# Optimization experiments

Measured on AMD Instinct MI355X. Metric: run time of the kernel, lower is better.

The kernel has to match this reference:

```python
import jax, jax.numpy as jnp
import numpy as np

B, N, C = 16, 4096, 512
FR = 2          # fr_ratio
NH = 8          # num_heads
CF = C // FR    # 256, q/k/v projection dim
HD = (C // NH) // FR  # 32, per-head dim after fr reduction
EPS = 1e-4


def _abs_clamp(t):
    # sign(t) * clamp(|t|, 1e-4, 1e4), as in the torch module's abs_clamp
    return jnp.sign(t) * jnp.clip(jnp.abs(t), 1e-4, 1e4)


def setup_inputs() -> dict:
    key = jax.random.key(0)
    ks = jax.random.split(key, 8)
    s = 0.02  # trunc_normal_(std=0.02) init scale
    return {
        "query": jax.random.normal(ks[0], (B, N, C), jnp.float32),
        "Wq": jax.random.normal(ks[1], (CF, C), jnp.float32) * s,
        "bq": jnp.zeros((CF,), jnp.float32),
        "Wk": jax.random.normal(ks[2], (CF, C), jnp.float32) * s,
        "bk": jnp.zeros((CF,), jnp.float32),
        "Wv": jax.random.normal(ks[3], (CF, C), jnp.float32) * s,
        "bv": jnp.zeros((CF,), jnp.float32),
        "Wo": jax.random.normal(ks[4], (C, CF), jnp.float32) * s,
        "bo": jnp.zeros((C,), jnp.float32),
        "Wse1": jax.random.normal(ks[5], (C // 2, C), jnp.float32) * s,
        "Wse2": jax.random.normal(ks[6], (C, C // 2), jnp.float32) * s,
        "H": 64,
        "W": 64,
    }


def reference(query, Wq, bq, Wk, bk, Wv, bv, Wo, bo, Wse1, Wse2, H, W):
    Bq, Nq, Cq = query.shape  # N == H*W
    # --- squeeze-excitation gate: mean over tokens -> 2-layer MLP -> sigmoid
    se = jnp.mean(query, axis=1)                                   # [B, C]
    se = jax.nn.sigmoid(jax.nn.relu(se @ Wse1.T) @ Wse2.T)         # [B, C]

    # --- q/k/v projections (sr_ratio=1: k/v from full-length query)
    q = jax.nn.relu(query @ Wq.T + bq).reshape(Bq, Nq, NH, HD)     # [B,N,h,d]
    k = jax.nn.relu(query @ Wk.T + bk).reshape(Bq, Nq, NH, HD)
    v = (query @ Wv.T + bv).reshape(Bq, Nq, NH, HD)

    # --- cosFormer-style 2D positional feature maps
    c = jnp.pi / 2
    idx = jnp.arange(Nq)
    a = (c * (idx // W).astype(query.dtype) / H)[None, :, None, None]  # row angle
    b = (c * (idx % W).astype(query.dtype) / W)[None, :, None, None]   # col angle
    q_ = jnp.concatenate([q * jnp.cos(a), q * jnp.sin(a),
                          q * jnp.cos(b), q * jnp.sin(b)], axis=-1)    # [B,N,h,4d]
    k_ = jnp.concatenate([k * jnp.cos(a), k * jnp.sin(a),
                          k * jnp.cos(b), k * jnp.sin(b)], axis=-1)    # sr_ratio=1 -> same angles

    # --- linear attention: kv state then q lookup, with abs-clamping
    kv = _abs_clamp(jnp.einsum('bnhf,bnhd->bhfd', k_, v))          # [B,h,4d,d]
    k_sum = jnp.sum(k_, axis=1, keepdims=True)                     # [B,1,h,4d]
    z = _abs_clamp(1.0 / (jnp.sum(q_ * k_sum, axis=-1) + EPS))     # [B,N,h]
    out = _abs_clamp(jnp.einsum('bnhf,bhfd->bnhd', q_, kv))        # [B,N,h,d]
    out = _abs_clamp(out * z[..., None])

    # --- output projection + SE residual gating
    out = _abs_clamp(out.reshape(Bq, Nq, CF) @ Wo.T + bo)          # [B,N,C]
    out = _abs_clamp(out + out * se[:, None, :])
    return out
```

## Files before the change

kernel.cpp:

```cpp
#include <hip/hip_runtime.h>
#include <math.h>

#define B_   16
#define N_   4096
#define C_   512
#define CF_  256
#define NH_  8
#define HD_  32
#define FHD_ 128
#define EPS_ 1e-4f
#define PI2F 1.5707963267948966f

typedef _Float16 half8 __attribute__((ext_vector_type(8)));
typedef _Float16 half4 __attribute__((ext_vector_type(4)));
typedef _Float16 half2v __attribute__((ext_vector_type(2)));
typedef float f32x4 __attribute__((ext_vector_type(4)));
typedef unsigned short u16x8 __attribute__((ext_vector_type(8)));

__device__ __forceinline__ float abs_clamp(float t) {
    float a = fminf(fmaxf(fabsf(t), 1e-4f), 1e4f);
    return t > 0.f ? a : (t < 0.f ? -a : 0.f);
}
__device__ __forceinline__ void gld16(const void* g, void* l) {
    __builtin_amdgcn_global_load_lds(
        (const __attribute__((address_space(1))) void*)g,
        (__attribute__((address_space(3))) void*)l, 16, 0, 0);
}

__global__ __launch_bounds__(256) void se_sum_kernel(const float* __restrict__ q,
                                                     float* __restrict__ sesum,
                                                     _Float16* __restrict__ q16) {
    int b = blockIdx.x, chunk = blockIdx.y;
    int t = threadIdx.x;
    int c0 = 2 * t;
    const float* p = q + ((size_t)b * N_ + (size_t)chunk * 256) * C_ + c0;
    _Float16* o = q16 + ((size_t)b * N_ + (size_t)chunk * 256) * C_ + c0;
    float a0 = 0.f, a1 = 0.f;
    for (int n = 0; n < 256; n++) {
        float2 v = *(const float2*)(p + (size_t)n * C_);
        a0 += v.x;
        a1 += v.y;
        half2v hv;
        hv[0] = (_Float16)v.x;
        hv[1] = (_Float16)v.y;
        *(half2v*)(o + (size_t)n * C_) = hv;
    }
    atomicAdd(&sesum[b * C_ + c0], a0);
    atomicAdd(&sesum[b * C_ + c0 + 1], a1);
}

__global__ __launch_bounds__(256) void se_gate_kernel(const float* __restrict__ sesum,
                                                      const float* __restrict__ Wse1,
                                                      const float* __restrict__ Wse2,
                                                      float* __restrict__ segate) {
    __shared__ float sm[C_];
    __shared__ float hm[C_ / 2];
    int b = blockIdx.x, t = threadIdx.x;
    sm[t]       = sesum[b * C_ + t]       * (1.f / N_);
    sm[t + 256] = sesum[b * C_ + t + 256] * (1.f / N_);
    __syncthreads();
    {
        const float* w = Wse1 + (size_t)t * C_;
        float acc = 0.f;
        for (int c2 = 0; c2 < C_; c2++) acc += sm[c2] * w[c2];
        hm[t] = fmaxf(acc, 0.f);
    }
    __syncthreads();
    for (int r = 0; r < 2; r++) {
        int c2 = t + r * 256;
        const float* w2 = Wse2 + (size_t)c2 * (C_ / 2);
        float a2 = 0.f;
        for (int j = 0; j < C_ / 2; j++) a2 += hm[j] * w2[j];
        segate[b * C_ + c2] = 1.f / (1.f + expf(-a2));
    }
}

__global__ __launch_bounds__(256) void convert_w(const float* __restrict__ Wq,
                                                 const float* __restrict__ Wk,
                                                 const float* __restrict__ Wv,
                                                 const float* __restrict__ Wo,
                                                 _Float16* __restrict__ wcat,
                                                 _Float16* __restrict__ wo16) {
    int i = blockIdx.x * 256 + threadIdx.x;
    if (i < 768 * 512) {
        int r = i >> 9, c = i & 511;
        float w = (r < 256) ? Wq[(size_t)r * 512 + c]
                : (r < 512) ? Wk[(size_t)(r - 256) * 512 + c]
                            : Wv[(size_t)(r - 512) * 512 + c];
        wcat[i] = (_Float16)w;
    } else {
        int j = i - 768 * 512;
        wo16[j] = (_Float16)Wo[j];
    }
}

__global__ __launch_bounds__(768) void gemm_qkv(
    const _Float16* __restrict__ A16, const _Float16* __restrict__ Bw,
    const float* __restrict__ bq, const float* __restrict__ bk, const float* __restrict__ bv,
    _Float16* __restrict__ O0, _Float16* __restrict__ O1, _Float16* __restrict__ O2) {
    constexpr int K = 512;
    constexpr int NITER = K / 32;

    __shared__ __align__(16) unsigned short As[2][128 * 32];
    __shared__ __align__(16) unsigned short Bs[2][384 * 32];

    const int t = threadIdx.x;
    const int Mb = blockIdx.y * 128;
    const int nrow0 = blockIdx.x * 384;

    const int lane = t & 63;
    const int wv = t >> 6;
    const int mq = (wv & 1) * 64;
    const int nq = (wv >> 1) * 64;
    const int mrow = lane & 15;
    const int kq = lane >> 4;
    const int fragoff = mrow * 32 + ((kq ^ ((mrow >> 1) & 3)) * 8);

    const unsigned char* bsrc0;
    const unsigned char* bsrc1;
    int boff0, boff1;
    {
        int cid0 = t, cid1 = t + 768;
        int m0 = cid0 >> 2, c0 = (cid0 & 3) ^ ((m0 >> 1) & 3);
        int m1 = cid1 >> 2, c1 = (cid1 & 3) ^ ((m1 >> 1) & 3);
        bsrc0 = (const unsigned char*)(Bw + (size_t)(nrow0 + m0) * K + c0 * 8);
        bsrc1 = (const unsigned char*)(Bw + (size_t)(nrow0 + m1) * K + c1 * 8);
        boff0 = cid0 * 8;
        boff1 = cid1 * 8;
    }
    const unsigned char* asrc = nullptr;
    int aoff = 0;
    if (t < 512) {
        int m0 = t >> 2, c0 = (t & 3) ^ ((m0 >> 1) & 3);
        asrc = (const unsigned char*)(A16 + (size_t)(Mb + m0) * K + c0 * 8);
        aoff = t * 8;
    }

    f32x4 acc[4][4];
#pragma unroll
    for (int mi = 0; mi < 4; mi++)
#pragma unroll
        for (int ni = 0; ni < 4; ni++) acc[mi][ni] = (f32x4){0.f, 0.f, 0.f, 0.f};

    if (t < 512) gld16(asrc, &As[0][aoff]);
    gld16(bsrc0, &Bs[0][boff0]);
    gld16(bsrc1, &Bs[0][boff1]);
    __syncthreads();

    int cur = 0;
#pragma unroll 1
    for (int it = 0; it < NITER; ++it) {
        if (it + 1 < NITER) {
            if (t < 512) gld16(asrc + (it + 1) * 64, &As[cur ^ 1][aoff]);
            gld16(bsrc0 + (it + 1) * 64, &Bs[cur ^ 1][boff0]);
            gld16(bsrc1 + (it + 1) * 64, &Bs[cur ^ 1][boff1]);
        }

        half8 ah[4], bh[4];
#pragma unroll
        for (int mi = 0; mi < 4; mi++)
            ah[mi] = *(const half8*)&As[cur][(mq + mi * 16) * 32 + fragoff];
#pragma unroll
        for (int ni = 0; ni < 4; ni++)
            bh[ni] = *(const half8*)&Bs[cur][(nq + ni * 16) * 32 + fragoff];
#pragma unroll
        for (int mi = 0; mi < 4; mi++)
#pragma unroll
            for (int ni = 0; ni < 4; ni++)
                acc[mi][ni] = __builtin_amdgcn_mfma_f32_16x16x32_f16(ah[mi], bh[ni], acc[mi][ni], 0, 0, 0);

        if (it + 1 < NITER) __syncthreads();
        cur ^= 1;
    }

#pragma unroll
    for (int ni = 0; ni < 4; ni++) {
        int gc = nrow0 + nq + ni * 16 + mrow;
        int mat = gc >> 8;
        int col = gc & 255;
        const float* bias = (mat == 0) ? bq : (mat == 1) ? bk : bv;
        _Float16* O = (mat == 0) ? O0 : (mat == 1) ? O1 : O2;
        float bb = bias[col];
#pragma unroll
        for (int mi = 0; mi < 4; mi++)
#pragma unroll
            for (int r = 0; r < 4; r++) {
                int m = Mb + mq + mi * 16 + kq * 4 + r;
                float v2 = acc[mi][ni][r] + bb;
                if (mat < 2) v2 = fmaxf(v2, 0.f);
                O[(size_t)m * CF_ + col] = (_Float16)v2;
            }
    }
}

__global__ __launch_bounds__(1024) void gemm_out(
    const _Float16* __restrict__ A16, const _Float16* __restrict__ Bw,
    const float* __restrict__ bo, const float* __restrict__ sg,
    float* __restrict__ Of) {
    constexpr int K = 256;
    constexpr int NITER = K / 32;

    __shared__ __align__(16) unsigned short As[2][128 * 32];
    __shared__ __align__(16) unsigned short Bs[2][512 * 32];

    const int t = threadIdx.x;
    const int Mb = blockIdx.x * 128;

    const int lane = t & 63;
    const int wv = t >> 6;
    const int mq = (wv & 1) * 64;
    const int nq = (wv >> 1) * 64;
    const int mrow = lane & 15;
    const int kq = lane >> 4;
    const int fragoff = mrow * 32 + ((kq ^ ((mrow >> 1) & 3)) * 8);

    const unsigned char* bsrc0;
    const unsigned char* bsrc1;
    int boff0, boff1;
    {
        int cid0 = t, cid1 = t + 1024;
        int m0 = cid0 >> 2, c0 = (cid0 & 3) ^ ((m0 >> 1) & 3);
        int m1 = cid1 >> 2, c1 = (cid1 & 3) ^ ((m1 >> 1) & 3);
        bsrc0 = (const unsigned char*)(Bw + (size_t)m0 * K + c0 * 8);
        bsrc1 = (const unsigned char*)(Bw + (size_t)m1 * K + c1 * 8);
        boff0 = cid0 * 8;
        boff1 = cid1 * 8;
    }
    const unsigned char* asrc = nullptr;
    int aoff = 0;
    if (t < 512) {
        int m0 = t >> 2, c0 = (t & 3) ^ ((m0 >> 1) & 3);
        asrc = (const unsigned char*)(A16 + (size_t)(Mb + m0) * K + c0 * 8);
        aoff = t * 8;
    }

    f32x4 acc[4][4];
#pragma unroll
    for (int mi = 0; mi < 4; mi++)
#pragma unroll
        for (int ni = 0; ni < 4; ni++) acc[mi][ni] = (f32x4){0.f, 0.f, 0.f, 0.f};

    if (t < 512) gld16(asrc, &As[0][aoff]);
    gld16(bsrc0, &Bs[0][boff0]);
    gld16(bsrc1, &Bs[0][boff1]);
    __syncthreads();

    int cur = 0;
#pragma unroll 1
    for (int it = 0; it < NITER; ++it) {
        if (it + 1 < NITER) {
            if (t < 512) gld16(asrc + (it + 1) * 64, &As[cur ^ 1][aoff]);
            gld16(bsrc0 + (it + 1) * 64, &Bs[cur ^ 1][boff0]);
            gld16(bsrc1 + (it + 1) * 64, &Bs[cur ^ 1][boff1]);
        }

        half8 ah[4], bh[4];
#pragma unroll
        for (int mi = 0; mi < 4; mi++)
            ah[mi] = *(const half8*)&As[cur][(mq + mi * 16) * 32 + fragoff];
#pragma unroll
        for (int ni = 0; ni < 4; ni++)
            bh[ni] = *(const half8*)&Bs[cur][(nq + ni * 16) * 32 + fragoff];
#pragma unroll
        for (int mi = 0; mi < 4; mi++)
#pragma unroll
            for (int ni = 0; ni < 4; ni++)
                acc[mi][ni] = __builtin_amdgcn_mfma_f32_16x16x32_f16(ah[mi], bh[ni], acc[mi][ni], 0, 0, 0);

        if (it + 1 < NITER) __syncthreads();
        cur ^= 1;
    }

    int b = Mb >> 12;
#pragma unroll
    for (int ni = 0; ni < 4; ni++) {
        int gc = nq + ni * 16 + mrow;
        float bb = bo[gc];
        float gv = sg[b * C_ + gc];
#pragma unroll
        for (int mi = 0; mi < 4; mi++)
#pragma unroll
            for (int r = 0; r < 4; r++) {
                int m = Mb + mq + mi * 16 + kq * 4 + r;
                float v2 = abs_clamp(acc[mi][ni][r] + bb);
                v2 = abs_clamp(v2 * (1.f + gv));
                Of[(size_t)m * C_ + gc] = v2;
            }
    }
}

__global__ __launch_bounds__(256) void kv_mfma_kernel(const _Float16* __restrict__ kin,
                                                      const _Float16* __restrict__ vin,
                                                      float* __restrict__ kvout,
                                                      float* __restrict__ ksum) {
    __shared__ __align__(16) unsigned short Ah[128 * 64];
    __shared__ __align__(16) unsigned short Bh[48 * 64];

    const int t = threadIdx.x;
    const int c8 = blockIdx.x;
    const int h = blockIdx.y, b = blockIdx.z;
    const int dp = t & 31;
    const int octet = t >> 5;

    if (t < 128) {
        int r = 32 + (t & 15);
        int oc = t >> 4;
        int off = r * 64 + (((oc ^ ((r >> 3) & 7)) & 7) * 8);
        unsigned short fill = (r == 32) ? (unsigned short)0x3C00 : (unsigned short)0;
        u16x8 z = {fill, fill, fill, fill, fill, fill, fill, fill};
        *(u16x8*)&Bh[off] = z;
    }

    float cbv[8], sbv[8];
#pragma unroll
    for (int i = 0; i < 8; i++) {
        float ang = (PI2F / 64.f) * (float)(octet * 8 + i);
        cbv[i] = cosf(ang);
        sbv[i] = sinf(ang);
    }

    const int lane = t & 63;
    const int wv = t >> 6;
    const int mrow = lane & 15;
    const int kq = lane >> 4;

    f32x4 acc[2][3];
#pragma unroll
    for (int mi = 0; mi < 2; mi++)
#pragma unroll
        for (int ni = 0; ni < 3; ni++) acc[mi][ni] = (f32x4){0.f, 0.f, 0.f, 0.f};

    int offA[4];
#pragma unroll
    for (int tvar = 0; tvar < 4; tvar++) {
        int f = tvar * 32 + dp;
        offA[tvar] = f * 64 + (((octet ^ ((f >> 3) & 7)) & 7) * 8);
    }
    const int offB = dp * 64 + (((octet ^ ((dp >> 3) & 7)) & 7) * 8);

#pragma unroll 1
    for (int ch = 0; ch < 8; ch++) {
        const int n0 = c8 * 512 + ch * 64;
        const int rrow = n0 >> 6;
        float aang = (PI2F / 64.f) * (float)rrow;
        float ca = cosf(aang), sa = sinf(aang);

        const _Float16* kp = kin + ((size_t)b * N_ + n0 + octet * 8) * CF_ + h * HD_ + dp;
        const _Float16* vp = vin + ((size_t)b * N_ + n0 + octet * 8) * CF_ + h * HD_ + dp;
        float kvl[8];
        _Float16 vvl[8];
#pragma unroll
        for (int i = 0; i < 8; i++) kvl[i] = (float)kp[(size_t)i * CF_];
#pragma unroll
        for (int i = 0; i < 8; i++) vvl[i] = vp[(size_t)i * CF_];

        __syncthreads();

#pragma unroll
        for (int tvar = 0; tvar < 4; tvar++) {
            half8 hv;
#pragma unroll
            for (int i = 0; i < 8; i++) {
                float val = kvl[i] * (tvar == 0 ? ca : tvar == 1 ? sa : tvar == 2 ? cbv[i] : sbv[i]);
                hv[i] = (_Float16)val;
            }
            *(half8*)&Ah[offA[tvar]] = hv;
        }
        {
            half8 hv;
#pragma unroll
            for (int i = 0; i < 8; i++) hv[i] = vvl[i];
            *(half8*)&Bh[offB] = hv;
        }
        __syncthreads();

#pragma unroll
        for (int s = 0; s < 2; s++) {
            half8 ah[2], bh[3];
            int koct = s * 4 + kq;
#pragma unroll
            for (int mi = 0; mi < 2; mi++) {
                int f = (wv * 2 + mi) * 16 + mrow;
                ah[mi] = *(const half8*)&Ah[f * 64 + (((koct ^ ((f >> 3) & 7)) & 7) * 8)];
            }
#pragma unroll
            for (int ni = 0; ni < 3; ni++) {
                int nr = ni * 16 + mrow;
                bh[ni] = *(const half8*)&Bh[nr * 64 + (((koct ^ ((nr >> 3) & 7)) & 7) * 8)];
            }
#pragma unroll
            for (int mi = 0; mi < 2; mi++)
#pragma unroll
                for (int ni = 0; ni < 3; ni++)
                    acc[mi][ni] = __builtin_amdgcn_mfma_f32_16x16x32_f16(ah[mi], bh[ni], acc[mi][ni], 0, 0, 0);
        }
    }

    float* kvp = kvout + (size_t)(b * NH_ + h) * FHD_ * HD_;
    float* ksp = ksum + (size_t)(b * NH_ + h) * FHD_;
#pragma unroll
    for (int mi = 0; mi < 2; mi++) {
        int mt = wv * 2 + mi;
#pragma unroll
        for (int r = 0; r < 4; r++) {
            int f = mt * 16 + kq * 4 + r;
            atomicAdd(&kvp[(size_t)f * HD_ + mrow], acc[mi][0][r]);
            atomicAdd(&kvp[(size_t)f * HD_ + 16 + mrow], acc[mi][1][r]);
            if (mrow == 0) atomicAdd(&ksp[f], acc[mi][2][r]);
        }
    }
}

__global__ __launch_bounds__(256) void attn_kernel(const _Float16* __restrict__ qbuf,
                                                   const float* __restrict__ kvin,
                                                   const float* __restrict__ ksum,
                                                   _Float16* __restrict__ ob) {
    int chunk = blockIdx.x;
    int h = blockIdx.y, b = blockIdx.z;
    int t = threadIdx.x;
    __shared__ float kvS[128][32];
    __shared__ float qS[128][33];
    __shared__ float tS[128][4];
    __shared__ float ksS[128];
    __shared__ float zS[128];
    int n0 = chunk * 128;

    const float* kvp = kvin + ((size_t)(b * NH_ + h)) * FHD_ * HD_;
#pragma unroll
    for (int r = 0; r < 16; r++) {
        int idx = t + r * 256;
        (&kvS[0][0])[idx] = abs_clamp(kvp[idx]);
    }
    if (t < 128) ksS[t] = ksum[(size_t)(b * NH_ + h) * FHD_ + t];
#pragma unroll
    for (int r = 0; r < 16; r++) {
        int idx = t + r * 256;
        int tok = idx >> 5, d = idx & 31;
        qS[tok][d] = (float)qbuf[((size_t)b * N_ + n0 + tok) * CF_ + h * HD_ + d];
    }
    if (t < 128) {
        int n = n0 + t;
        float ra = (float)(n >> 6), cb = (float)(n & 63);
        float aa = (PI2F * ra) / 64.0f;
        float ab = (PI2F * cb) / 64.0f;
        tS[t][0] = cosf(aa); tS[t][1] = sinf(aa);
        tS[t][2] = cosf(ab); tS[t][3] = sinf(ab);
    }
    __syncthreads();
    if (t < 128) {
        float s = 0.f;
        for (int f = 0; f < 128; f++) s += qS[t][f & 31] * tS[t][f >> 5] * ksS[f];
        zS[t] = abs_clamp(1.f / (s + EPS_));
    }
    __syncthreads();

    int tx = t & 7, ty = t >> 3;
    float acc[4][4];
#pragma unroll
    for (int u = 0; u < 4; u++)
#pragma unroll
        for (int w = 0; w < 4; w++) acc[u][w] = 0.f;

#pragma unroll
    for (int ti = 0; ti < 4; ti++) {
        float tr0 = tS[ty * 4 + 0][ti];
        float tr1 = tS[ty * 4 + 1][ti];
        float tr2 = tS[ty * 4 + 2][ti];
        float tr3 = tS[ty * 4 + 3][ti];
        for (int dd = 0; dd < 32; dd++) {
            int f = ti * 32 + dd;
            float4 kvv = *(const float4*)&kvS[f][tx * 4];
            float q0 = qS[ty * 4 + 0][dd] * tr0;
            float q1 = qS[ty * 4 + 1][dd] * tr1;
            float q2 = qS[ty * 4 + 2][dd] * tr2;
            float q3 = qS[ty * 4 + 3][dd] * tr3;
            acc[0][0] += q0 * kvv.x; acc[0][1] += q0 * kvv.y; acc[0][2] += q0 * kvv.z; acc[0][3] += q0 * kvv.w;
            acc[1][0] += q1 * kvv.x; acc[1][1] += q1 * kvv.y; acc[1][2] += q1 * kvv.z; acc[1][3] += q1 * kvv.w;
            acc[2][0] += q2 * kvv.x; acc[2][1] += q2 * kvv.y; acc[2][2] += q2 * kvv.z; acc[2][3] += q2 * kvv.w;
            acc[3][0] += q3 * kvv.x; acc[3][1] += q3 * kvv.y; acc[3][2] += q3 * kvv.z; acc[3][3] += q3 * kvv.w;
        }
    }

#pragma unroll
    for (int u = 0; u < 4; u++) {
        int tok = ty * 4 + u;
        float z = zS[tok];
        half4 hv;
        hv[0] = (_Float16)abs_clamp(abs_clamp(acc[u][0]) * z);
        hv[1] = (_Float16)abs_clamp(abs_clamp(acc[u][1]) * z);
        hv[2] = (_Float16)abs_clamp(abs_clamp(acc[u][2]) * z);
        hv[3] = (_Float16)abs_clamp(abs_clamp(acc[u][3]) * z);
        size_t base = ((size_t)b * N_ + n0 + tok) * CF_ + h * HD_ + tx * 4;
        *(half4*)&ob[base] = hv;
    }
}

extern "C" void kernel_launch(void* const* d_in, const int* in_sizes, int n_in,
                              void* d_out, int out_size, void* d_ws, size_t ws_size,
                              hipStream_t stream) {
    (void)in_sizes; (void)n_in; (void)out_size; (void)ws_size;
    const float* query = (const float*)d_in[0];
    const float* Wq = (const float*)d_in[1];
    const float* bq = (const float*)d_in[2];
    const float* Wk = (const float*)d_in[3];
    const float* bk = (const float*)d_in[4];
    const float* Wv = (const float*)d_in[5];
    const float* bv = (const float*)d_in[6];
    const float* Wo = (const float*)d_in[7];
    const float* bo = (const float*)d_in[8];
    const float* Wse1 = (const float*)d_in[9];
    const float* Wse2 = (const float*)d_in[10];
    float* out = (float*)d_out;

    unsigned char* ws = (unsigned char*)d_ws;
    const size_t MB = 1024ull * 1024ull;
    _Float16* q16 = (_Float16*)(ws + 0);
    _Float16* ob  = (_Float16*)(ws + 0);
    _Float16* qb = (_Float16*)(ws + 64 * MB);
    _Float16* kb = (_Float16*)(ws + 96 * MB);
    _Float16* vb = (_Float16*)(ws + 128 * MB);
    _Float16* wcat = (_Float16*)(ws + 160 * MB);
    _Float16* wo16 = (_Float16*)(ws + 160 * MB + 786432);
    float* kvb = (float*)(ws + 161 * MB);
    float* ksb = (float*)(ws + 163 * MB);
    float* ssb = (float*)(ws + 163 * MB + 65536);
    float* sgb = (float*)(ws + 163 * MB + 98304);

    hipMemsetAsync(kvb, 0, 2097152 + 65536 + 32768, stream);

    convert_w<<<2048, 256, 0, stream>>>(Wq, Wk, Wv, Wo, wcat, wo16);
    se_sum_kernel<<<dim3(B_, 16), 256, 0, stream>>>(query, ssb, q16);
    se_gate_kernel<<<B_, 256, 0, stream>>>(ssb, Wse1, Wse2, sgb);
    gemm_qkv<<<dim3(2, 512), 768, 0, stream>>>(q16, wcat, bq, bk, bv, qb, kb, vb);
    kv_mfma_kernel<<<dim3(8, NH_, B_), 256, 0, stream>>>(kb, vb, kvb, ksb);
    attn_kernel<<<dim3(32, NH_, B_), 256, 0, stream>>>(qb, kvb, ksb, ob);
    gemm_out<<<512, 1024, 0, stream>>>(ob, wo16, bo, sgb, out);
}
```

Measured before the change: 565.4 us.

## Rewrite attention lookup kernel with fp16 MFMA and fused k_sum normalizer

The per-chunk attention kernel now builds the positional-feature q tile in swizzled fp16 shared memory and runs q_·kv as 16x16x32 MFMA ops instead of scalar FP32 FMAs. k_sum is appended as an extra row of the B operand, so the z normalizer comes out of the same MFMA pass. The kv accumulator layout is transposed to d-major to match the new B operand loading. This removes the scalar FMA loop and the serial z reduction, at the cost of fp16 rounding on q_, kv and k_sum.

```diff
diff --git a/kernel.cpp b/kernel.cpp
--- a/kernel.cpp
+++ b/kernel.cpp
@@ -404,8 +404,8 @@
 #pragma unroll
         for (int r = 0; r < 4; r++) {
             int f = mt * 16 + kq * 4 + r;
-            atomicAdd(&kvp[(size_t)f * HD_ + mrow], acc[mi][0][r]);
-            atomicAdd(&kvp[(size_t)f * HD_ + 16 + mrow], acc[mi][1][r]);
+            atomicAdd(&kvp[(size_t)mrow * FHD_ + f], acc[mi][0][r]);
+            atomicAdd(&kvp[(size_t)(16 + mrow) * FHD_ + f], acc[mi][1][r]);
             if (mrow == 0) atomicAdd(&ksp[f], acc[mi][2][r]);
         }
     }
@@ -415,83 +415,126 @@
                                                    const float* __restrict__ kvin,
                                                    const float* __restrict__ ksum,
                                                    _Float16* __restrict__ ob) {
-    int chunk = blockIdx.x;
-    int h = blockIdx.y, b = blockIdx.z;
-    int t = threadIdx.x;
-    __shared__ float kvS[128][32];
-    __shared__ float qS[128][33];
-    __shared__ float tS[128][4];
-    __shared__ float ksS[128];
+    __shared__ __align__(16) unsigned short Aq[128 * 128];
+    __shared__ __align__(16) unsigned short Bk[48 * 128];
     __shared__ float zS[128];
-    int n0 = chunk * 128;
-
-    const float* kvp = kvin + ((size_t)(b * NH_ + h)) * FHD_ * HD_;
-#pragma unroll
-    for (int r = 0; r < 16; r++) {
-        int idx = t + r * 256;
-        (&kvS[0][0])[idx] = abs_clamp(kvp[idx]);
-    }
-    if (t < 128) ksS[t] = ksum[(size_t)(b * NH_ + h) * FHD_ + t];
-#pragma unroll
-    for (int r = 0; r < 16; r++) {
-        int idx = t + r * 256;
-        int tok = idx >> 5, d = idx & 31;
-        qS[tok][d] = (float)qbuf[((size_t)b * N_ + n0 + tok) * CF_ + h * HD_ + d];
-    }
-    if (t < 128) {
-        int n = n0 + t;
-        float ra = (float)(n >> 6), cb = (float)(n & 63);
-        float aa = (PI2F * ra) / 64.0f;
-        float ab = (PI2F * cb) / 64.0f;
-        tS[t][0] = cosf(aa); tS[t][1] = sinf(aa);
-        tS[t][2] = cosf(ab); tS[t][3] = sinf(ab);
+
+    const int chunk = blockIdx.x;
+    const int h = blockIdx.y, b = blockIdx.z;
+    const int t = threadIdx.x;
+    const int n0 = chunk * 128;
+
+    {
+        const float* kvp = kvin + ((size_t)(b * NH_ + h)) * (HD_ * FHD_);
+        int d = t >> 3;
+        int c0 = (t & 7) * 2;
+#pragma unroll
+        for (int cc = 0; cc < 2; cc++) {
+            int c = c0 + cc;
+            const float* src = kvp + (size_t)d * FHD_ + c * 8;
+            half8 hv;
+#pragma unroll
+            for (int i = 0; i < 8; i++) hv[i] = (_Float16)abs_clamp(src[i]);
+            *(half8*)&Bk[d * 128 + ((c ^ (d & 7)) * 8)] = hv;
+        }
+        if (t < 16) {
+            const float* ks = ksum + ((size_t)(b * NH_ + h)) * FHD_ + t * 8;
+            half8 hv;
+#pragma unroll
+            for (int i = 0; i < 8; i++) hv[i] = (_Float16)ks[i];
+            *(half8*)&Bk[32 * 128 + (t * 8)] = hv;
+        } else {
+            int idx = t - 16;
+            int r = 33 + (idx >> 4), c = idx & 15;
+            half8 z = {};
+            *(half8*)&Bk[r * 128 + ((c ^ (r & 7)) * 8)] = z;
+        }
+    }
+    {
+        int tok = t >> 1, hf = t & 1;
+        int n = n0 + tok;
+        const _Float16* qp = qbuf + ((size_t)b * N_ + n) * CF_ + h * HD_;
+        half8 q0 = *(const half8*)(qp + 0);
+        half8 q1 = *(const half8*)(qp + 8);
+        half8 q2 = *(const half8*)(qp + 16);
+        half8 q3 = *(const half8*)(qp + 24);
+        float f0, f1;
+        if (hf == 0) {
+            float aa = (PI2F / 64.f) * (float)(n >> 6);
+            f0 = cosf(aa); f1 = sinf(aa);
+        } else {
+            float ab = (PI2F / 64.f) * (float)(n & 63);
+            f0 = cosf(ab); f1 = sinf(ab);
+        }
+#pragma unroll
+        for (int ti = 0; ti < 2; ti++) {
+            float fac = ti ? f1 : f0;
+#pragma unroll
+            for (int dc = 0; dc < 4; dc++) {
+                half8 qv = (dc == 0) ? q0 : (dc == 1) ? q1 : (dc == 2) ? q2 : q3;
+                half8 hv;
+#pragma unroll
+                for (int i = 0; i < 8; i++) hv[i] = (_Float16)((float)qv[i] * fac);
+                int c = hf * 8 + ti * 4 + dc;
+                *(half8*)&Aq[tok * 128 + ((c ^ (tok & 7)) * 8)] = hv;
+            }
+        }
     }
     __syncthreads();
-    if (t < 128) {
-        float s = 0.f;
-        for (int f = 0; f < 128; f++) s += qS[t][f & 31] * tS[t][f >> 5] * ksS[f];
-        zS[t] = abs_clamp(1.f / (s + EPS_));
+
+    const int lane = t & 63;
+    const int wv = t >> 6;
+    const int mrow = lane & 15;
+    const int kq = lane >> 4;
+
+    f32x4 acc[2][3];
+#pragma unroll
+    for (int mi = 0; mi < 2; mi++)
+#pragma unroll
+        for (int ni = 0; ni < 3; ni++) acc[mi][ni] = (f32x4){0.f, 0.f, 0.f, 0.f};
+
+#pragma unroll
+    for (int ks = 0; ks < 4; ks++) {
+        half8 ah[2], bh[3];
+        int cpos = ks * 4 + kq;
+#pragma unroll
+        for (int mi = 0; mi < 2; mi++) {
+            int row = wv * 32 + mi * 16 + mrow;
+            ah[mi] = *(const half8*)&Aq[row * 128 + ((cpos ^ (row & 7)) * 8)];
+        }
+#pragma unroll
+        for (int ni = 0; ni < 3; ni++) {
+            int row = ni * 16 + mrow;
+            bh[ni] = *(const half8*)&Bk[row * 128 + ((cpos ^ (row & 7)) * 8)];
+        }
+#pragma unroll
+        for (int mi = 0; mi < 2; mi++)
+#pragma unroll
+            for (int ni = 0; ni < 3; ni++)
+                acc[mi][ni] = __builtin_amdgcn_mfma_f32_16x16x32_f16(ah[mi], bh[ni], acc[mi][ni], 0, 0, 0);
+    }
+
+    if (mrow == 0) {
+#pragma unroll
+        for (int mi = 0; mi < 2; mi++)
+#pragma unroll
+            for (int r = 0; r < 4; r++)
+                zS[wv * 32 + mi * 16 + kq * 4 + r] = acc[mi][2][r];
     }
     __syncthreads();
 
-    int tx = t & 7, ty = t >> 3;
-    float acc[4][4];
-#pragma unroll
-    for (int u = 0; u < 4; u++)
-#pragma unroll
-        for (int w = 0; w < 4; w++) acc[u][w] = 0.f;
-
-#pragma unroll
-    for (int ti = 0; ti < 4; ti++) {
-        float tr0 = tS[ty * 4 + 0][ti];
-        float tr1 = tS[ty * 4 + 1][ti];
-        float tr2 = tS[ty * 4 + 2][ti];
-        float tr3 = tS[ty * 4 + 3][ti];
-        for (int dd = 0; dd < 32; dd++) {
-            int f = ti * 32 + dd;
-            float4 kvv = *(const float4*)&kvS[f][tx * 4];
-            float q0 = qS[ty * 4 + 0][dd] * tr0;
-            float q1 = qS[ty * 4 + 1][dd] * tr1;
-            float q2 = qS[ty * 4 + 2][dd] * tr2;
-            float q3 = qS[ty * 4 + 3][dd] * tr3;
-            acc[0][0] += q0 * kvv.x; acc[0][1] += q0 * kvv.y; acc[0][2] += q0 * kvv.z; acc[0][3] += q0 * kvv.w;
-            acc[1][0] += q1 * kvv.x; acc[1][1] += q1 * kvv.y; acc[1][2] += q1 * kvv.z; acc[1][3] += q1 * kvv.w;
-            acc[2][0] += q2 * kvv.x; acc[2][1] += q2 * kvv.y; acc[2][2] += q2 * kvv.z; acc[2][3] += q2 * kvv.w;
-            acc[3][0] += q3 * kvv.x; acc[3][1] += q3 * kvv.y; acc[3][2] += q3 * kvv.z; acc[3][3] += q3 * kvv.w;
-        }
-    }
-
-#pragma unroll
-    for (int u = 0; u < 4; u++) {
-        int tok = ty * 4 + u;
-        float z = zS[tok];
-        half4 hv;
-        hv[0] = (_Float16)abs_clamp(abs_clamp(acc[u][0]) * z);
-        hv[1] = (_Float16)abs_clamp(abs_clamp(acc[u][1]) * z);
-        hv[2] = (_Float16)abs_clamp(abs_clamp(acc[u][2]) * z);
-        hv[3] = (_Float16)abs_clamp(abs_clamp(acc[u][3]) * z);
-        size_t base = ((size_t)b * N_ + n0 + tok) * CF_ + h * HD_ + tx * 4;
-        *(half4*)&ob[base] = hv;
+#pragma unroll
+    for (int mi = 0; mi < 2; mi++) {
+#pragma unroll
+        for (int r = 0; r < 4; r++) {
+            int tok = wv * 32 + mi * 16 + kq * 4 + r;
+            float z = abs_clamp(1.f / (zS[tok] + EPS_));
+            float v0 = abs_clamp(abs_clamp(acc[mi][0][r]) * z);
+            float v1 = abs_clamp(abs_clamp(acc[mi][1][r]) * z);
+            size_t base = ((size_t)b * N_ + n0 + tok) * CF_ + h * HD_;
+            ob[base + mrow] = (_Float16)v0;
+            ob[base + 16 + mrow] = (_Float16)v1;
+        }
     }
 }
 
```

Result: faster. 533.3 us (-5.7%).
